# Performance work log

Measured on AMD Instinct MI355X. Metric: run time of the kernel, lower is better.

The kernel has to match this reference:

```python
import jax, jax.numpy as jnp
import numpy as np

# Static configuration (mirrors MeshPotential.__init__ + mesh-size derivation)
SIGMA = 1.0          # atomic_gaussian_width
SPACING = 0.2        # mesh_spacing
ORDER = 4            # interpolation_order (cubic, P3M M4 assignment)
L = 10.0             # cubic cell edge used in setup_inputs
N_ATOMS = 200000
# ns = 2**ceil(log2(2*L/SPACING + 1)) = 2**ceil(log2(101)) = 128 per axis
NX = NY = NZ = 128


def setup_inputs() -> dict:
    key = jax.random.key(0)
    k1, k2 = jax.random.split(key)
    cell = L * jnp.eye(3, dtype=jnp.float32)                  # (3,3) cell rows = basis vectors
    positions = jax.random.uniform(k1, (N_ATOMS, 3), jnp.float32, 0.0, L)
    charges = jax.random.normal(k2, (N_ATOMS, 1), jnp.float32)
    return {"cell": cell, "positions": positions, "charges": charges}


def _interp(cell, positions):
    """Order-4 (cubic B-spline / P3M) interpolation weights + flat mesh indices."""
    ns = jnp.array([NX, NY, NZ], dtype=positions.dtype)
    rel = (positions @ jnp.linalg.inv(cell)) * ns             # (n,3) fractional * mesh size
    idx0 = jnp.floor(rel).astype(jnp.int32)                   # even order: floor-based stencil
    x = rel - (idx0.astype(rel.dtype) + 0.5)                  # offset in [-1/2, 1/2)
    x2, x3 = x * x, x * x * x
    # P3M charge-assignment weights of order 4, grid points [floor-1, floor, floor+1, floor+2]
    w = jnp.stack([
        1.0 - 6.0 * x + 12.0 * x2 - 8.0 * x3,
        23.0 - 30.0 * x - 12.0 * x2 + 24.0 * x3,
        23.0 + 30.0 * x - 12.0 * x2 - 24.0 * x3,
        1.0 + 6.0 * x + 12.0 * x2 + 8.0 * x3,
    ]) / 48.0                                                 # (4, n, 3)
    shifts = jnp.array([-1, 0, 1, 2], dtype=jnp.int32)
    idx = (idx0[None] + shifts[:, None, None]) % jnp.array([NX, NY, NZ], jnp.int32)  # (4,n,3)
    ix, iy, iz = idx[..., 0], idx[..., 1], idx[..., 2]        # (4,n) each
    flat = (ix[:, None, None] * NY + iy[None, :, None]) * NZ + iz[None, None, :]     # (4,4,4,n)
    flat = flat.reshape(64, -1).T                             # (n,64) flat mesh indices
    w3d = jnp.einsum('ia,ja,ka->aijk', w[..., 0], w[..., 1], w[..., 2]).reshape(-1, 64)  # (n,64)
    return w3d, flat


def _forward(cell, positions, charges):
    n, C = charges.shape
    w3d, flat = _interp(cell, positions)
    # points_to_mesh: spline-weighted scatter of charges onto the mesh
    vals = charges.T[:, :, None] * w3d[None]                  # (C,n,64)
    rho = jnp.zeros((C, NX * NY * NZ), charges.dtype).at[:, flat].add(vals)
    rho = rho.reshape(C, NX, NY, NZ)
    # Fourier-space convolution with G(k^2) = 4*pi/k^2 * exp(-sigma^2 k^2 / 2), G(0)=0
    Brec = 2.0 * jnp.pi * jnp.linalg.inv(cell).T              # rows = reciprocal vectors b_i
    mx = jnp.fft.fftfreq(NX) * NX
    my = jnp.fft.fftfreq(NY) * NY
    mz = jnp.fft.rfftfreq(NZ) * NZ
    kvec = (mx[:, None, None, None] * Brec[0]
            + my[None, :, None, None] * Brec[1]
            + mz[None, None, :, None] * Brec[2])              # (NX,NY,NZ//2+1,3)
    ksq = jnp.sum(kvec * kvec, axis=-1).astype(charges.dtype)
    safe = jnp.where(ksq == 0.0, 1.0, ksq)
    G = jnp.where(ksq == 0.0, 0.0, 4.0 * jnp.pi / safe * jnp.exp(-0.5 * SIGMA * SIGMA * safe))
    rho_hat = jnp.fft.rfftn(rho, axes=(1, 2, 3))              # unnormalized forward FFT
    pot_mesh = jnp.fft.irfftn(rho_hat * G, s=(NX, NY, NZ), axes=(1, 2, 3), norm="forward")
    pot_mesh = pot_mesh / jnp.abs(jnp.linalg.det(cell))       # divide by cell volume
    # mesh_to_points: spline-weighted gather back to atom positions
    gathered = pot_mesh.reshape(C, -1)[:, flat] * w3d[None]   # (C,n,64)
    potential = gathered.sum(-1).T                            # (n,C)
    # subtract self-contribution of the atom-centered gaussian
    potential = potential - charges * (jnp.sqrt(2.0 / jnp.pi) / SIGMA)
    return potential


def reference(cell, positions, charges):
    return _forward(cell, positions, charges)
```

## Files before the change

### kernel.cpp

```cpp
#include <hip/hip_runtime.h>
#include <math.h>

#define NTOT (128*128*128)
#define NBIN2 64
#define BINS (NBIN2*NBIN2*NBIN2)
#define SCAN_BLOCKS 256

#define ZP 72
#define CAP 1024

#define PI_F      3.14159265358979323846f
#define TWO_PI_F  6.28318530717958647692f
#define FOUR_PI_F 12.5663706143591729539f


__device__ inline void inv3x3(const float* __restrict__ c, float* inv, float* detOut) {
    float a = c[0], b = c[1], cc = c[2];
    float d = c[3], e = c[4], f  = c[5];
    float g = c[6], h = c[7], i  = c[8];
    float A = e * i - f * h;
    float B = f * g - d * i;
    float C = d * h - e * g;
    float det = a * A + b * B + cc * C;
    float r = 1.0f / det;
    inv[0] = A * r;              inv[1] = (cc * h - b * i) * r;  inv[2] = (b * f - cc * e) * r;
    inv[3] = B * r;              inv[4] = (a * i - cc * g) * r;  inv[5] = (cc * d - a * f) * r;
    inv[6] = C * r;              inv[7] = (b * g - a * h) * r;   inv[8] = (a * e - b * d) * r;
    *detOut = det;
}

__device__ inline void atom_rel(const float* __restrict__ cell,
                                const float* __restrict__ pos, int t,
                                float* rx, float* ry, float* rz) {
    float inv[9]; float det;
    inv3x3(cell, inv, &det);
    float px = pos[3 * t], py = pos[3 * t + 1], pz = pos[3 * t + 2];
    *rx = (px * inv[0] + py * inv[3] + pz * inv[6]) * 128.0f;
    *ry = (px * inv[1] + py * inv[4] + pz * inv[7]) * 128.0f;
    *rz = (px * inv[2] + py * inv[5] + pz * inv[8]) * 128.0f;
}

__device__ inline int bin_of(float rx, float ry, float rz) {
    int ix = ((int)floorf(rx)) & 127;
    int iy = ((int)floorf(ry)) & 127;
    int iz = ((int)floorf(rz)) & 127;
    return ((((ix >> 1) << 6) | (iy >> 1)) << 6) | (iz >> 1);
}

__device__ inline float wrap128(float u) {
    u = (u > 64.0f) ? u - 128.0f : u;
    u = (u < -64.0f) ? u + 128.0f : u;
    return u;
}

__device__ inline float bspline(float u) {
    float a = fabsf(u);
    float t = fmaxf(2.0f - a, 0.0f);
    float s = fmaxf(1.0f - a, 0.0f);
    return t * t * t - 4.0f * s * s * s;
}


__global__ void zero_int_kernel(int* __restrict__ p, int n) {
    int i = blockIdx.x * blockDim.x + threadIdx.x;
    if (i < n) p[i] = 0;
}

__global__ void hist_kernel(const float* __restrict__ cell, const float* __restrict__ pos,
                            int* __restrict__ hist, int n) {
    int t = blockIdx.x * blockDim.x + threadIdx.x;
    if (t >= n) return;
    float rx, ry, rz;
    atom_rel(cell, pos, t, &rx, &ry, &rz);
    atomicAdd(&hist[bin_of(rx, ry, rz)], 1);
}

__global__ __launch_bounds__(256) void scan_local(const int4* __restrict__ hist4,
                                                  int4* __restrict__ off4,
                                                  int* __restrict__ partials) {
    const int b = blockIdx.x, t = threadIdx.x;
    const int idx = b * 256 + t;
    int4 h = hist4[idx];
    int s = h.x + h.y + h.z + h.w;
    int lane = t & 63, wv = t >> 6;
    int v = s;
    #pragma unroll
    for (int d = 1; d < 64; d <<= 1) {
        int o = __shfl_up(v, d, 64);
        if (lane >= d) v += o;
    }
    __shared__ int wsum[4];
    if (lane == 63) wsum[wv] = v;
    __syncthreads();
    int add = 0;
    #pragma unroll
    for (int k = 0; k < 4; ++k) if (k < wv) add += wsum[k];
    int run = add + v - s;
    int4 o4;
    o4.x = run; run += h.x;
    o4.y = run; run += h.y;
    o4.z = run; run += h.z;
    o4.w = run; run += h.w;
    off4[idx] = o4;
    if (t == 255) partials[b] = run;
}

__global__ __launch_bounds__(256) void scan_add(int4* __restrict__ hist4,
                                                int4* __restrict__ off4,
                                                const int* __restrict__ partials,
                                                int* __restrict__ offsets) {
    const int b = blockIdx.x, t = threadIdx.x;
    int lane = t & 63, wv = t >> 6;
    int v = (t < b) ? partials[t] : 0;
    #pragma unroll
    for (int d = 32; d >= 1; d >>= 1) v += __shfl_xor(v, d, 64);
    __shared__ int ws2[4];
    __shared__ int base_s;
    if (lane == 0) ws2[wv] = v;
    __syncthreads();
    if (t == 0) base_s = ws2[0] + ws2[1] + ws2[2] + ws2[3];
    __syncthreads();
    const int base = base_s;
    const int idx = b * 256 + t;
    int4 o4 = off4[idx];
    o4.x += base; o4.y += base; o4.z += base; o4.w += base;
    off4[idx]  = o4;
    hist4[idx] = o4;
    if (b == SCAN_BLOCKS - 1 && t == 255) offsets[BINS] = base + partials[b];
}

__global__ void reorder_kernel(const float* __restrict__ cell, const float* __restrict__ pos,
                               const float* __restrict__ q, int* __restrict__ cursor,
                               float4* __restrict__ sorted, int* __restrict__ sortedIdx, int n) {
    int t = blockIdx.x * blockDim.x + threadIdx.x;
    if (t >= n) return;
    float rx, ry, rz;
    atom_rel(cell, pos, t, &rx, &ry, &rz);
    int p = atomicAdd(&cursor[bin_of(rx, ry, rz)], 1);
    sorted[p] = make_float4(rx, ry, rz, q[t]);
    sortedIdx[p] = t;
}


__global__ __launch_bounds__(512) void lds_scatter_kernel(const float4* __restrict__ atoms,
                                                          const int* __restrict__ offsets,
                                                          float* __restrict__ rmesh) {
    const int blk = blockIdx.x;
    const int bz = blk & 7, by = (blk >> 3) & 7, bx = blk >> 6;
    const int ox = bx << 4, oy = by << 4, oz = bz << 4;
    const int gbx0 = ((ox - 2) & 127) >> 1;
    const int gby0 = ((oy - 2) & 127) >> 1;
    const int gbz0 = ((oz - 2) & 127) >> 1;

    __shared__ float4 satoms[CAP];
    __shared__ int P[1025];
    __shared__ int wsum[8];

    const int t = threadIdx.x;

    int c0 = 0, c1 = 0, g0 = 0, g1 = 0;
    {
        int b = 2 * t;
        if (b < 1000) {
            int jx = b / 100, rr = b - jx * 100, jy = rr / 10, jz = rr - jy * 10;
            int gb = ((((gbx0 + jx) & 63) << 6) | ((gby0 + jy) & 63)) << 6 | ((gbz0 + jz) & 63);
            g0 = offsets[gb]; c0 = offsets[gb + 1] - g0;
        }
        b = 2 * t + 1;
        if (b < 1000) {
            int jx = b / 100, rr = b - jx * 100, jy = rr / 10, jz = rr - jy * 10;
            int gb = ((((gbx0 + jx) & 63) << 6) | ((gby0 + jy) & 63)) << 6 | ((gbz0 + jz) & 63);
            g1 = offsets[gb]; c1 = offsets[gb + 1] - g1;
        }
    }

    int s = c0 + c1;
    int lane = t & 63, wv = t >> 6;
    int v = s;
    #pragma unroll
    for (int d = 1; d < 64; d <<= 1) {
        int o = __shfl_up(v, d, 64);
        if (lane >= d) v += o;
    }
    if (lane == 63) wsum[wv] = v;
    __syncthreads();
    int add = 0;
    #pragma unroll
    for (int k = 0; k < 8; ++k) if (k < wv) add += wsum[k];
    const int pre = add + v - s;
    P[2 * t] = pre;
    P[2 * t + 1] = pre + c0;
    if (t == 511) P[1024] = add + v;
    __syncthreads();

    for (int k = 0; k < c0; ++k) {
        int d = pre + k;
        if (d >= CAP) break;
        satoms[d] = atoms[g0 + k];
    }
    {
        int pre1 = pre + c0;
        for (int k = 0; k < c1; ++k) {
            int d = pre1 + k;
            if (d >= CAP) break;
            satoms[d] = atoms[g1 + k];
        }
    }
    __syncthreads();

    const int qz = t & 7, qy = (t >> 3) & 7, qx = t >> 6;
    const int cx0 = ox + (qx << 1), cy0 = oy + (qy << 1), cz0 = oz + (qz << 1);
    const float fcx = (float)cx0, fcy = (float)cy0, fcz = (float)cz0;

    float a000 = 0.0f, a001 = 0.0f, a010 = 0.0f, a011 = 0.0f;
    float a100 = 0.0f, a101 = 0.0f, a110 = 0.0f, a111 = 0.0f;

    int r = -1, i = 0, e = 0;
    while (i >= e) {
        if (++r >= 9) break;
        int dbx = r / 3, dby = r - dbx * 3;
        int bin0 = ((qx + dbx) * 10 + (qy + dby)) * 10 + qz;
        i = P[bin0];
        e = P[bin0 + 3];
        if (e > CAP) e = CAP;
    }
    while (r < 9) {
        float4 a = satoms[i];

        float ux = wrap128(a.x - fcx);
        float wx0 = bspline(ux);
        float wx1 = bspline(ux - 1.0f);
        float uy = wrap128(a.y - fcy);
        float wy0 = bspline(uy);
        float wy1 = bspline(uy - 1.0f);
        float uz = wrap128(a.z - fcz);
        float wz0 = bspline(uz);
        float wz1 = bspline(uz - 1.0f);
        float qs = a.w * (1.0f / 216.0f);
        float qx0 = qs * wx0, qx1 = qs * wx1;
        float m00 = qx0 * wy0, m01 = qx0 * wy1;
        float m10 = qx1 * wy0, m11 = qx1 * wy1;
        a000 += m00 * wz0; a001 += m00 * wz1;
        a010 += m01 * wz0; a011 += m01 * wz1;
        a100 += m10 * wz0; a101 += m10 * wz1;
        a110 += m11 * wz0; a111 += m11 * wz1;

        if (++i >= e) {
            while (i >= e) {
                if (++r >= 9) break;
                int dbx = r / 3, dby = r - dbx * 3;
                int bin0 = ((qx + dbx) * 10 + (qy + dby)) * 10 + qz;
                i = P[bin0];
                e = P[bin0 + 3];
                if (e > CAP) e = CAP;
            }
            if (r >= 9) break;
        }
    }

    *(float2*)&rmesh[((size_t)cx0       << 14) | ((size_t)cy0       << 7) | (size_t)cz0] = make_float2(a000, a001);
    *(float2*)&rmesh[((size_t)cx0       << 14) | ((size_t)(cy0 + 1) << 7) | (size_t)cz0] = make_float2(a010, a011);
    *(float2*)&rmesh[((size_t)(cx0 + 1) << 14) | ((size_t)cy0       << 7) | (size_t)cz0] = make_float2(a100, a101);
    *(float2*)&rmesh[((size_t)(cx0 + 1) << 14) | ((size_t)(cy0 + 1) << 7) | (size_t)cz0] = make_float2(a110, a111);
}


__global__ __launch_bounds__(512) void lds_gather_kernel(const float4* __restrict__ atoms,
                                                         const int* __restrict__ sortedIdx,
                                                         const int* __restrict__ offsets,
                                                         const float* __restrict__ rmesh,
                                                         float* __restrict__ out) {
    const int blk = blockIdx.x;
    const int bz = blk & 7, by = (blk >> 3) & 7, bx = blk >> 6;
    const int ox = bx << 4, oy = by << 4, oz = bz << 4;

    __shared__ float tile[19][19][20];
    __shared__ int P[513];
    __shared__ int gbase[512];
    __shared__ int wsum[8];

    const int t = threadIdx.x;

    for (int u = t; u < 19 * 19 * 19; u += 512) {
        int dz = u % 19, rest = u / 19;
        int dy = rest % 19, dx = rest / 19;
        int gx = (ox - 1 + dx) & 127;
        int gy = (oy - 1 + dy) & 127;
        int gz = (oz - 1 + dz) & 127;
        tile[dx][dy][dz] = rmesh[((size_t)gx << 14) | ((size_t)gy << 7) | (size_t)gz];
    }

    int cnt;
    {
        int uz = t & 7, uy = (t >> 3) & 7, ux = t >> 6;
        int gb = ((((bx << 3) | ux) << 6) | ((by << 3) | uy)) << 6 | ((bz << 3) | uz);
        int s0 = offsets[gb];
        gbase[t] = s0;
        cnt = offsets[gb + 1] - s0;
    }
    int lane = t & 63, wv = t >> 6;
    int v = cnt;
    #pragma unroll
    for (int d = 1; d < 64; d <<= 1) {
        int o = __shfl_up(v, d, 64);
        if (lane >= d) v += o;
    }
    if (lane == 63) wsum[wv] = v;
    __syncthreads();
    int add = 0;
    #pragma unroll
    for (int k = 0; k < 8; ++k) if (k < wv) add += wsum[k];
    P[t] = add + v - cnt;
    if (t == 511) P[512] = add + v;
    __syncthreads();

    const int total = P[512];
    for (int i = t; i < total; i += 512) {
        int lo = 0, hi = 511;
        #pragma unroll
        for (int st = 0; st < 9; ++st) {
            int mid = (lo + hi + 1) >> 1;
            if (P[mid] <= i) lo = mid; else hi = mid - 1;
        }
        const int j = lo;
        const int src = gbase[j] + (i - P[j]);
        float4 a = atoms[src];

        float flx = floorf(a.x), fly = floorf(a.y), flz = floorf(a.z);
        int lx = (((int)flx) & 127) - ox + 1;
        int ly = (((int)fly) & 127) - oy + 1;
        int lz = (((int)flz) & 127) - oz + 1;
        float xx = a.x - flx, yy = a.y - fly, zz = a.z - flz;

        float wx0 = bspline(xx + 1.0f), wx1 = bspline(xx);
        float wx2 = bspline(xx - 1.0f), wx3 = bspline(xx - 2.0f);
        float wy0 = bspline(yy + 1.0f), wy1 = bspline(yy);
        float wy2 = bspline(yy - 1.0f), wy3 = bspline(yy - 2.0f);
        float wz0 = bspline(zz + 1.0f), wz1 = bspline(zz);
        float wz2 = bspline(zz - 1.0f), wz3 = bspline(zz - 2.0f);

        float sum = 0.0f;
        #pragma unroll
        for (int di = 0; di < 4; ++di) {
            float wxv = (di == 0) ? wx0 : (di == 1) ? wx1 : (di == 2) ? wx2 : wx3;
            const float* rowx = &tile[lx - 1 + di][0][0];
            float sy = 0.0f;
            #pragma unroll
            for (int dj = 0; dj < 4; ++dj) {
                float wyv = (dj == 0) ? wy0 : (dj == 1) ? wy1 : (dj == 2) ? wy2 : wy3;
                const float* rowz = rowx + (ly - 1 + dj) * 20 + (lz - 1);
                float sz = wz0 * rowz[0] + wz1 * rowz[1] + wz2 * rowz[2] + wz3 * rowz[3];
                sy += wyv * sz;
            }
            sum += wxv * sy;
        }
        out[sortedIdx[src]] = sum * (1.0f / 216.0f) - a.w * 0.79788456080286535588f;
    }
}


__device__ inline void bfly_dif(float& rr, float& ii, int h, bool hi, float cs, float sn) {
    float pr = __shfl_xor(rr, h), pi = __shfl_xor(ii, h);
    float br = hi ? (pr - rr) : (rr + pr);
    float bi = hi ? (pi - ii) : (ii + pi);
    rr = cs * br - sn * bi;
    ii = cs * bi + sn * br;
}

__device__ inline void bfly_dit(float& rr, float& ii, int h, bool hi, float cs, float sn) {
    float pr = __shfl_xor(rr, h), pi = __shfl_xor(ii, h);
    float xr = hi ? rr : pr, xi = hi ? ii : pi;
    float br = hi ? pr : rr, bi = hi ? pi : ii;
    float tr = cs * xr - sn * xi, ti = cs * xi + sn * xr;
    rr = hi ? (br - tr) : (br + tr);
    ii = hi ? (bi - ti) : (bi + ti);
}

__device__ inline void wfft_dif_fwd(float& r0, float& i0, float& r1, float& i1, int lane) {
    {
        float ang = -PI_F * (float)lane * (1.0f / 64.0f);
        float sn, cs; __sincosf(ang, &sn, &cs);
        float ar = r0 + r1, ai = i0 + i1;
        float dr = r0 - r1, di = i0 - i1;
        r0 = ar; i0 = ai;
        r1 = cs * dr - sn * di;
        i1 = cs * di + sn * dr;
    }
    #pragma unroll
    for (int h = 32; h >= 1; h >>= 1) {
        int pos = lane & (h - 1);
        bool hi = (lane & h) != 0;
        float ang = hi ? (-PI_F * (float)pos / (float)h) : 0.0f;
        float sn, cs; __sincosf(ang, &sn, &cs);
        bfly_dif(r0, i0, h, hi, cs, sn);
        bfly_dif(r1, i1, h, hi, cs, sn);
    }
}

__device__ inline void wfft_dit_inv(float& r0, float& i0, float& r1, float& i1, int lane) {
    #pragma unroll
    for (int h = 1; h <= 32; h <<= 1) {
        int pos = lane & (h - 1);
        bool hi = (lane & h) != 0;
        float ang = PI_F * (float)pos / (float)h;
        float sn, cs; __sincosf(ang, &sn, &cs);
        bfly_dit(r0, i0, h, hi, cs, sn);
        bfly_dit(r1, i1, h, hi, cs, sn);
    }
    {
        float ang = PI_F * (float)lane * (1.0f / 64.0f);
        float sn, cs; __sincosf(ang, &sn, &cs);
        float tr = cs * r1 - sn * i1, ti = cs * i1 + sn * r1;
        float nr = r0 + tr, ni = i0 + ti;
        r1 = r0 - tr; i1 = i0 - ti;
        r0 = nr; i0 = ni;
    }
}


__global__ __launch_bounds__(1024) void fftZfwd(const float* __restrict__ rin,
                                                float2* __restrict__ mesh) {
    __shared__ float tre[16][132], tim[16][132];
    const int t = threadIdx.x, b = blockIdx.x;
    for (int u = t; u < 2048; u += 1024) {
        int l = u >> 7, e = u & 127;
        tre[l][e] = rin[((size_t)((b << 4) | l) << 7) + e];
    }
    __syncthreads();
    const int w = t >> 6, lane = t & 63;
    float r0 = tre[w][lane],      i0 = 0.0f;
    float r1 = tre[w][lane + 64], i1 = 0.0f;
    wfft_dif_fwd(r0, i0, r1, i1, lane);
    int e0 = (int)(__brev((unsigned)lane) >> 25);
    tre[w][e0] = r0;     tim[w][e0] = i0;
    tre[w][e0 + 1] = r1; tim[w][e0 + 1] = i1;
    __syncthreads();
    for (int u = t; u < 2048; u += 1024) {
        int l = u >> 7, e = u & 127;
        if (e < ZP)
            mesh[(size_t)((b << 4) | l) * ZP + e] = make_float2(tre[l][e], tim[l][e]);
    }
}


__global__ __launch_bounds__(512) void fftYfwd(float2* __restrict__ mesh) {
    __shared__ float tre[8][132], tim[8][132];
    const int t = threadIdx.x, b = blockIdx.x;
    const int x = b & 127, zf0 = (b >> 7) << 3;
    const size_t rb = ((size_t)(x << 7)) * ZP + zf0;
    for (int u = t; u < 1024; u += 512) {
        int e = u >> 3, dz = u & 7;
        float2 vv = mesh[rb + (size_t)e * ZP + dz];
        tre[dz][e] = vv.x; tim[dz][e] = vv.y;
    }
    __syncthreads();
    const int w = t >> 6, lane = t & 63;
    float r0 = tre[w][lane],      i0 = tim[w][lane];
    float r1 = tre[w][lane + 64], i1 = tim[w][lane + 64];
    wfft_dif_fwd(r0, i0, r1, i1, lane);
    tre[w][lane] = r0;      tim[w][lane] = i0;
    tre[w][lane + 64] = r1; tim[w][lane + 64] = i1;
    __syncthreads();
    for (int u = t; u < 1024; u += 512) {
        int e = u >> 3, dz = u & 7;
        mesh[rb + (size_t)e * ZP + dz] = make_float2(tre[dz][e], tim[dz][e]);
    }
}


__global__ __launch_bounds__(512) void fftXGw(float2* __restrict__ mesh,
                                              const float* __restrict__ cell) {
    __shared__ float tre[8][132], tim[8][132];
    const int t = threadIdx.x, b = blockIdx.x;
    const int py = b & 127, zf0 = (b >> 7) << 3;
    for (int u = t; u < 1024; u += 512) {
        int e = u >> 3, dz = u & 7;
        float2 vv = mesh[(size_t)((e << 7) | py) * ZP + zf0 + dz];
        tre[dz][e] = vv.x; tim[dz][e] = vv.y;
    }
    __syncthreads();
    const int w = t >> 6, lane = t & 63;
    float r0 = tre[w][lane],      i0 = tim[w][lane];
    float r1 = tre[w][lane + 64], i1 = tim[w][lane + 64];
    wfft_dif_fwd(r0, i0, r1, i1, lane);
    {
        float inv[9]; float det; inv3x3(cell, inv, &det);
        float invVol = 1.0f / fabsf(det);
        int my = (int)(__brev((unsigned)py) >> 25);
        int mz = zf0 + w;
        float fy = (my < 64) ? (float)my : (float)(my - 128);
        float fz = (mz < 64) ? (float)mz : (float)(mz - 128);
        int mx0 = (int)(__brev((unsigned)lane) >> 25);
        #pragma unroll
        for (int s = 0; s < 2; ++s) {
            int mx = mx0 + s;
            float fx = (mx < 64) ? (float)mx : (float)(mx - 128);
            float kx = TWO_PI_F * (fx * inv[0] + fy * inv[1] + fz * inv[2]);
            float ky = TWO_PI_F * (fx * inv[3] + fy * inv[4] + fz * inv[5]);
            float kz = TWO_PI_F * (fx * inv[6] + fy * inv[7] + fz * inv[8]);
            float ksq = kx * kx + ky * ky + kz * kz;
            float G = (ksq == 0.0f) ? 0.0f
                      : FOUR_PI_F / ksq * __expf(-0.5f * ksq) * invVol;
            if (s == 0) { r0 *= G; i0 *= G; } else { r1 *= G; i1 *= G; }
        }
    }
    wfft_dit_inv(r0, i0, r1, i1, lane);
    tre[w][lane] = r0;      tim[w][lane] = i0;
    tre[w][lane + 64] = r1; tim[w][lane + 64] = i1;
    __syncthreads();
    for (int u = t; u < 1024; u += 512) {
        int e = u >> 3, dz = u & 7;
        mesh[(size_t)((e << 7) | py) * ZP + zf0 + dz] =
            make_float2(tre[dz][e], tim[dz][e]);
    }
}


__global__ __launch_bounds__(512) void fftYinv(float2* __restrict__ mesh) {
    __shared__ float tre[8][132], tim[8][132];
    const int t = threadIdx.x, b = blockIdx.x;
    const int x = b & 127, zf0 = (b >> 7) << 3;
    const size_t rb = ((size_t)(x << 7)) * ZP + zf0;
    for (int u = t; u < 1024; u += 512) {
        int e = u >> 3, dz = u & 7;
        float2 vv = mesh[rb + (size_t)e * ZP + dz];
        tre[dz][e] = vv.x; tim[dz][e] = vv.y;
    }
    __syncthreads();
    const int w = t >> 6, lane = t & 63;
    float r0 = tre[w][lane],      i0 = tim[w][lane];
    float r1 = tre[w][lane + 64], i1 = tim[w][lane + 64];
    wfft_dit_inv(r0, i0, r1, i1, lane);
    tre[w][lane] = r0;      tim[w][lane] = i0;
    tre[w][lane + 64] = r1; tim[w][lane + 64] = i1;
    __syncthreads();
    for (int u = t; u < 1024; u += 512) {
        int e = u >> 3, dz = u & 7;
        mesh[rb + (size_t)e * ZP + dz] = make_float2(tre[dz][e], tim[dz][e]);
    }
}


__global__ __launch_bounds__(1024) void fftZinv(const float2* __restrict__ mesh,
                                                float* __restrict__ rout) {
    __shared__ float tre[16][132], tim[16][132];
    const int t = threadIdx.x, b = blockIdx.x;
    for (int u = t; u < 2048; u += 1024) {
        int l = u >> 7, e = u & 127;
        int src = (e <= 64) ? e : 128 - e;
        float2 vv = mesh[(size_t)((b << 4) | l) * ZP + src];
        tre[l][e] = vv.x;
        tim[l][e] = (e <= 64) ? vv.y : -vv.y;
    }
    __syncthreads();
    const int w = t >> 6, lane = t & 63;
    int e0 = (int)(__brev((unsigned)lane) >> 25);
    float r0 = tre[w][e0],     i0 = tim[w][e0];
    float r1 = tre[w][e0 + 1], i1 = tim[w][e0 + 1];
    wfft_dit_inv(r0, i0, r1, i1, lane);
    const size_t rb = ((size_t)((b << 4) | w) << 7);
    rout[rb + lane] = r0;
    rout[rb + lane + 64] = r1;
}


extern "C" void kernel_launch(void* const* d_in, const int* in_sizes, int n_in,
                              void* d_out, int out_size, void* d_ws, size_t ws_size,
                              hipStream_t stream) {
    const float* cell = (const float*)d_in[0];
    const float* pos  = (const float*)d_in[1];
    const float* q    = (const float*)d_in[2];
    float* out = (float*)d_out;
    const int n = in_sizes[2];

    char* ws = (char*)d_ws;
    size_t o = 0;
    float4* sorted   = (float4*)(ws + o); o += (size_t)n * 16;
    int* sortedIdx   = (int*)(ws + o);    o += (size_t)n * 4;  o = (o + 255) & ~(size_t)255;
    int* hist        = (int*)(ws + o);    o += (size_t)BINS * 4;
    int* offsets     = (int*)(ws + o);    o += (size_t)(BINS + 4) * 4;
    int* partials    = (int*)(ws + o);    o += (size_t)SCAN_BLOCKS * 4; o = (o + 255) & ~(size_t)255;
    float2* mesh     = (float2*)(ws + o); o += (size_t)128 * 128 * ZP * 8;
    float* rmesh     = (float*)(ws + o);

    zero_int_kernel<<<BINS / 256, 256, 0, stream>>>(hist, BINS);
    hist_kernel<<<(n + 255) / 256, 256, 0, stream>>>(cell, pos, hist, n);
    scan_local<<<SCAN_BLOCKS, 256, 0, stream>>>((const int4*)hist, (int4*)offsets, partials);
    scan_add<<<SCAN_BLOCKS, 256, 0, stream>>>((int4*)hist, (int4*)offsets, partials, offsets);
    reorder_kernel<<<(n + 255) / 256, 256, 0, stream>>>(cell, pos, q, hist, sorted, sortedIdx, n);

    lds_scatter_kernel<<<512, 512, 0, stream>>>(sorted, offsets, rmesh);

    fftZfwd<<<1024, 1024, 0, stream>>>(rmesh, mesh);
    fftYfwd<<<9 * 128, 512, 0, stream>>>(mesh);
    fftXGw<<<9 * 128, 512, 0, stream>>>(mesh, cell);
    fftYinv<<<9 * 128, 512, 0, stream>>>(mesh);
    fftZinv<<<1024, 1024, 0, stream>>>(mesh, rmesh);

    lds_gather_kernel<<<512, 512, 0, stream>>>(sorted, sortedIdx, offsets, rmesh, out);
}
```

Measured before the change: 135.7 us.

## Fuse Y/X FFT passes and Green's multiply into one per-z-plane LDS kernel

```diff
diff --git a/kernel.cpp b/kernel.cpp
--- a/kernel.cpp
+++ b/kernel.cpp
@@ -6,12 +6,14 @@
 #define BINS (NBIN2*NBIN2*NBIN2)
 #define SCAN_BLOCKS 256
 
-#define ZP 72
+#define NZF 65
 #define CAP 1024
 
 #define PI_F      3.14159265358979323846f
 #define TWO_PI_F  6.28318530717958647692f
 #define FOUR_PI_F 12.5663706143591729539f
+
+__device__ inline int rev7(int v) { return (int)(__brev((unsigned)v) >> 25); }
 
 
 __device__ inline void inv3x3(const float* __restrict__ c, float* inv, float* detOut) {
@@ -431,112 +433,88 @@
     float r0 = tre[w][lane],      i0 = 0.0f;
     float r1 = tre[w][lane + 64], i1 = 0.0f;
     wfft_dif_fwd(r0, i0, r1, i1, lane);
-    int e0 = (int)(__brev((unsigned)lane) >> 25);
+    int e0 = rev7(lane);
     tre[w][e0] = r0;     tim[w][e0] = i0;
     tre[w][e0 + 1] = r1; tim[w][e0 + 1] = i1;
     __syncthreads();
-    for (int u = t; u < 2048; u += 1024) {
-        int l = u >> 7, e = u & 127;
-        if (e < ZP)
-            mesh[(size_t)((b << 4) | l) * ZP + e] = make_float2(tre[l][e], tim[l][e]);
-    }
-}
-
-
-__global__ __launch_bounds__(512) void fftYfwd(float2* __restrict__ mesh) {
-    __shared__ float tre[8][132], tim[8][132];
-    const int t = threadIdx.x, b = blockIdx.x;
-    const int x = b & 127, zf0 = (b >> 7) << 3;
-    const size_t rb = ((size_t)(x << 7)) * ZP + zf0;
-    for (int u = t; u < 1024; u += 512) {
-        int e = u >> 3, dz = u & 7;
-        float2 vv = mesh[rb + (size_t)e * ZP + dz];
-        tre[dz][e] = vv.x; tim[dz][e] = vv.y;
-    }
-    __syncthreads();
+    for (int u = t; u < 16 * NZF; u += 1024) {
+        int l = u & 15, e = u >> 4;
+        mesh[((size_t)e << 14) + (size_t)((b << 4) | l)] = make_float2(tre[l][e], tim[l][e]);
+    }
+}
+
+
+__global__ __launch_bounds__(1024) void fftPlane(float2* __restrict__ mesh,
+                                                 const float* __restrict__ cell) {
+    __shared__ float sre[128][129], sim[128][129];
+    const int zf = blockIdx.x;
+    const int t = threadIdx.x;
+    const size_t base = (size_t)zf << 14;
+
+    for (int u = t; u < 16384; u += 1024) {
+        float2 v = mesh[base + u];
+        sre[u >> 7][u & 127] = v.x;
+        sim[u >> 7][u & 127] = v.y;
+    }
+    __syncthreads();
+
     const int w = t >> 6, lane = t & 63;
-    float r0 = tre[w][lane],      i0 = tim[w][lane];
-    float r1 = tre[w][lane + 64], i1 = tim[w][lane + 64];
-    wfft_dif_fwd(r0, i0, r1, i1, lane);
-    tre[w][lane] = r0;      tim[w][lane] = i0;
-    tre[w][lane + 64] = r1; tim[w][lane + 64] = i1;
-    __syncthreads();
-    for (int u = t; u < 1024; u += 512) {
-        int e = u >> 3, dz = u & 7;
-        mesh[rb + (size_t)e * ZP + dz] = make_float2(tre[dz][e], tim[dz][e]);
-    }
-}
-
-
-__global__ __launch_bounds__(512) void fftXGw(float2* __restrict__ mesh,
-                                              const float* __restrict__ cell) {
-    __shared__ float tre[8][132], tim[8][132];
-    const int t = threadIdx.x, b = blockIdx.x;
-    const int py = b & 127, zf0 = (b >> 7) << 3;
-    for (int u = t; u < 1024; u += 512) {
-        int e = u >> 3, dz = u & 7;
-        float2 vv = mesh[(size_t)((e << 7) | py) * ZP + zf0 + dz];
-        tre[dz][e] = vv.x; tim[dz][e] = vv.y;
-    }
-    __syncthreads();
-    const int w = t >> 6, lane = t & 63;
-    float r0 = tre[w][lane],      i0 = tim[w][lane];
-    float r1 = tre[w][lane + 64], i1 = tim[w][lane + 64];
-    wfft_dif_fwd(r0, i0, r1, i1, lane);
+
+    #pragma unroll 2
+    for (int k = 0; k < 8; ++k) {
+        int x = (k << 4) | w;
+        float r0 = sre[x][lane],      i0 = sim[x][lane];
+        float r1 = sre[x][lane + 64], i1 = sim[x][lane + 64];
+        wfft_dif_fwd(r0, i0, r1, i1, lane);
+        sre[x][lane] = r0;      sim[x][lane] = i0;
+        sre[x][lane + 64] = r1; sim[x][lane + 64] = i1;
+    }
+    __syncthreads();
+
     {
         float inv[9]; float det; inv3x3(cell, inv, &det);
         float invVol = 1.0f / fabsf(det);
-        int my = (int)(__brev((unsigned)py) >> 25);
-        int mz = zf0 + w;
-        float fy = (my < 64) ? (float)my : (float)(my - 128);
-        float fz = (mz < 64) ? (float)mz : (float)(mz - 128);
-        int mx0 = (int)(__brev((unsigned)lane) >> 25);
-        #pragma unroll
-        for (int s = 0; s < 2; ++s) {
-            int mx = mx0 + s;
-            float fx = (mx < 64) ? (float)mx : (float)(mx - 128);
-            float kx = TWO_PI_F * (fx * inv[0] + fy * inv[1] + fz * inv[2]);
-            float ky = TWO_PI_F * (fx * inv[3] + fy * inv[4] + fz * inv[5]);
-            float kz = TWO_PI_F * (fx * inv[6] + fy * inv[7] + fz * inv[8]);
-            float ksq = kx * kx + ky * ky + kz * kz;
-            float G = (ksq == 0.0f) ? 0.0f
-                      : FOUR_PI_F / ksq * __expf(-0.5f * ksq) * invVol;
-            if (s == 0) { r0 *= G; i0 *= G; } else { r1 *= G; i1 *= G; }
-        }
-    }
-    wfft_dit_inv(r0, i0, r1, i1, lane);
-    tre[w][lane] = r0;      tim[w][lane] = i0;
-    tre[w][lane + 64] = r1; tim[w][lane + 64] = i1;
-    __syncthreads();
-    for (int u = t; u < 1024; u += 512) {
-        int e = u >> 3, dz = u & 7;
-        mesh[(size_t)((e << 7) | py) * ZP + zf0 + dz] =
-            make_float2(tre[dz][e], tim[dz][e]);
-    }
-}
-
-
-__global__ __launch_bounds__(512) void fftYinv(float2* __restrict__ mesh) {
-    __shared__ float tre[8][132], tim[8][132];
-    const int t = threadIdx.x, b = blockIdx.x;
-    const int x = b & 127, zf0 = (b >> 7) << 3;
-    const size_t rb = ((size_t)(x << 7)) * ZP + zf0;
-    for (int u = t; u < 1024; u += 512) {
-        int e = u >> 3, dz = u & 7;
-        float2 vv = mesh[rb + (size_t)e * ZP + dz];
-        tre[dz][e] = vv.x; tim[dz][e] = vv.y;
-    }
-    __syncthreads();
-    const int w = t >> 6, lane = t & 63;
-    float r0 = tre[w][lane],      i0 = tim[w][lane];
-    float r1 = tre[w][lane + 64], i1 = tim[w][lane + 64];
-    wfft_dit_inv(r0, i0, r1, i1, lane);
-    tre[w][lane] = r0;      tim[w][lane] = i0;
-    tre[w][lane + 64] = r1; tim[w][lane + 64] = i1;
-    __syncthreads();
-    for (int u = t; u < 1024; u += 512) {
-        int e = u >> 3, dz = u & 7;
-        mesh[rb + (size_t)e * ZP + dz] = make_float2(tre[dz][e], tim[dz][e]);
+        float fz = (zf < 64) ? (float)zf : (float)(zf - 128);
+        int mx0 = rev7(lane);
+        for (int k = 0; k < 8; ++k) {
+            int py = (k << 4) | w;
+            float r0 = sre[lane][py],      i0 = sim[lane][py];
+            float r1 = sre[lane + 64][py], i1 = sim[lane + 64][py];
+            wfft_dif_fwd(r0, i0, r1, i1, lane);
+            int my = rev7(py);
+            float fy = (my < 64) ? (float)my : (float)(my - 128);
+            #pragma unroll
+            for (int s = 0; s < 2; ++s) {
+                int mx = mx0 + s;
+                float fx = (mx < 64) ? (float)mx : (float)(mx - 128);
+                float kx = TWO_PI_F * (fx * inv[0] + fy * inv[1] + fz * inv[2]);
+                float ky = TWO_PI_F * (fx * inv[3] + fy * inv[4] + fz * inv[5]);
+                float kz = TWO_PI_F * (fx * inv[6] + fy * inv[7] + fz * inv[8]);
+                float ksq = kx * kx + ky * ky + kz * kz;
+                float G = (ksq == 0.0f) ? 0.0f
+                          : FOUR_PI_F / ksq * __expf(-0.5f * ksq) * invVol;
+                if (s == 0) { r0 *= G; i0 *= G; } else { r1 *= G; i1 *= G; }
+            }
+            wfft_dit_inv(r0, i0, r1, i1, lane);
+            sre[lane][py] = r0;      sim[lane][py] = i0;
+            sre[lane + 64][py] = r1; sim[lane + 64][py] = i1;
+        }
+    }
+    __syncthreads();
+
+    #pragma unroll 2
+    for (int k = 0; k < 8; ++k) {
+        int x = (k << 4) | w;
+        float r0 = sre[x][lane],      i0 = sim[x][lane];
+        float r1 = sre[x][lane + 64], i1 = sim[x][lane + 64];
+        wfft_dit_inv(r0, i0, r1, i1, lane);
+        sre[x][lane] = r0;      sim[x][lane] = i0;
+        sre[x][lane + 64] = r1; sim[x][lane + 64] = i1;
+    }
+    __syncthreads();
+
+    for (int u = t; u < 16384; u += 1024) {
+        mesh[base + u] = make_float2(sre[u >> 7][u & 127], sim[u >> 7][u & 127]);
     }
 }
 
@@ -546,15 +524,15 @@
     __shared__ float tre[16][132], tim[16][132];
     const int t = threadIdx.x, b = blockIdx.x;
     for (int u = t; u < 2048; u += 1024) {
-        int l = u >> 7, e = u & 127;
+        int l = u & 15, e = u >> 4;
         int src = (e <= 64) ? e : 128 - e;
-        float2 vv = mesh[(size_t)((b << 4) | l) * ZP + src];
+        float2 vv = mesh[((size_t)src << 14) + (size_t)((b << 4) | l)];
         tre[l][e] = vv.x;
         tim[l][e] = (e <= 64) ? vv.y : -vv.y;
     }
     __syncthreads();
     const int w = t >> 6, lane = t & 63;
-    int e0 = (int)(__brev((unsigned)lane) >> 25);
+    int e0 = rev7(lane);
     float r0 = tre[w][e0],     i0 = tim[w][e0];
     float r1 = tre[w][e0 + 1], i1 = tim[w][e0 + 1];
     wfft_dit_inv(r0, i0, r1, i1, lane);
@@ -580,7 +558,7 @@
     int* hist        = (int*)(ws + o);    o += (size_t)BINS * 4;
     int* offsets     = (int*)(ws + o);    o += (size_t)(BINS + 4) * 4;
     int* partials    = (int*)(ws + o);    o += (size_t)SCAN_BLOCKS * 4; o = (o + 255) & ~(size_t)255;
-    float2* mesh     = (float2*)(ws + o); o += (size_t)128 * 128 * ZP * 8;
+    float2* mesh     = (float2*)(ws + o); o += (size_t)NZF * 16384 * 8;
     float* rmesh     = (float*)(ws + o);
 
     zero_int_kernel<<<BINS / 256, 256, 0, stream>>>(hist, BINS);
@@ -592,9 +570,7 @@
     lds_scatter_kernel<<<512, 512, 0, stream>>>(sorted, offsets, rmesh);
 
     fftZfwd<<<1024, 1024, 0, stream>>>(rmesh, mesh);
-    fftYfwd<<<9 * 128, 512, 0, stream>>>(mesh);
-    fftXGw<<<9 * 128, 512, 0, stream>>>(mesh, cell);
-    fftYinv<<<9 * 128, 512, 0, stream>>>(mesh);
+    fftPlane<<<NZF, 1024, 0, stream>>>(mesh, cell);
     fftZinv<<<1024, 1024, 0, stream>>>(mesh, rmesh);
 
     lds_gather_kernel<<<512, 512, 0, stream>>>(sorted, sortedIdx, offsets, rmesh, out);
```

After: 151.1 us. 11.3% more time.
